# Optimization experiments

Hardware: AMD Instinct MI355X
Metric: run time of the kernel (lower is better)

## Reference

```python
import jax, jax.numpy as jnp
import numpy as np

B, T, H = 2048, 2048, 32  # batch, sequence steps (columns of input), hidden size


def setup_inputs() -> dict:
    key = jax.random.key(0)
    ks = jax.random.split(key, 5)
    stdv = 1.0 / np.sqrt(H)
    u = lambda k, shp: jax.random.uniform(k, shp, jnp.float32, -stdv, stdv)
    return {
        "x": jax.random.normal(ks[0], (B, T), jnp.float32),
        "weight_ih": u(ks[1], (4 * H, 1)),
        "weight_hh": u(ks[2], (4 * H, H)),
        "bias_ih": u(ks[3], (4 * H,)),
        "bias_hh": u(ks[4], (4 * H,)),
    }


def reference(x, weight_ih, weight_hh, bias_ih, bias_hh):
    Bn, Tn = x.shape
    Hn = weight_hh.shape[1]
    xs = x.T[:, :, None]              # (T, B, 1): step-major inputs
    bias = bias_ih + bias_hh          # (4H,)

    def step(carry, x_t):
        h, c = carry                  # (B, H) each
        gates = x_t @ weight_ih.T + h @ weight_hh.T + bias  # (B, 4H)
        i, f, g, o = jnp.split(gates, 4, axis=1)
        i = jax.nn.sigmoid(i)
        f = jax.nn.sigmoid(f)
        g = jnp.tanh(g)
        o = jax.nn.sigmoid(o)
        # row 0 of the original skips the forget term entirely; with c0 = 0,
        # f * c0 == 0, so this is identical math.
        c_new = f * c + i * g
        h_new = o * jnp.tanh(c_new)
        return (h_new, c_new), h_new

    h0 = jnp.zeros((Bn, Hn), x.dtype)
    c0 = jnp.zeros((Bn, Hn), x.dtype)
    _, ys = jax.lax.scan(step, (h0, c0), xs)   # ys: (T, B, H)
    # torch.cat(h_matrix, 1): step-major blocks of width H along dim 1
    return jnp.transpose(ys, (1, 0, 2)).reshape(Bn, Tn * Hn)
```

## Files before the change

### kernel.cpp

```cpp
#include <hip/hip_runtime.h>
#include <hip/hip_fp16.h>


#define Bsz 2048
#define Tsz 2048
#define Hsz 32

typedef _Float16 v2h __attribute__((ext_vector_type(2)));

__device__ __forceinline__ float fast_rcp(float x) { return __builtin_amdgcn_rcpf(x); }
__device__ __forceinline__ float fast_exp2(float x) { return __builtin_amdgcn_exp2f(x); }

__device__ __forceinline__ float fdot2(unsigned a, unsigned b, float c) {
#if __has_builtin(__builtin_amdgcn_fdot2)
    return __builtin_amdgcn_fdot2(__builtin_bit_cast(v2h, a),
                                  __builtin_bit_cast(v2h, b), c, false);
#else
    v2h av = __builtin_bit_cast(v2h, a), bv = __builtin_bit_cast(v2h, b);
    return __fmaf_rn((float)av.x, (float)bv.x,
                     __fmaf_rn((float)av.y, (float)bv.y, c));
#endif
}

__device__ __forceinline__ void plswap(float a, float b, float& r0, float& r1) {
#if __has_builtin(__builtin_amdgcn_permlane32_swap)
    auto r = __builtin_amdgcn_permlane32_swap(__float_as_uint(a), __float_as_uint(b),
                                              false, false);
    r0 = __uint_as_float(r[0]);
    r1 = __uint_as_float(r[1]);
#else
    const bool hi = (threadIdx.x & 32) != 0;
    r0 = hi ? __shfl_xor(b, 32) : a;
    r1 = hi ? b : __shfl_xor(a, 32);
#endif
}

__device__ __forceinline__ unsigned pkh(float a, float b) {
    unsigned ua = (unsigned)__builtin_bit_cast(unsigned short, (_Float16)a);
    unsigned ub = (unsigned)__builtin_bit_cast(unsigned short, (_Float16)b);
    return ua | (ub << 16);
}

__global__ void lstm_prep_kernel(const float* __restrict__ w_ih,
                                 const float* __restrict__ w_hh,
                                 const float* __restrict__ b_ih,
                                 const float* __restrict__ b_hh,
                                 unsigned* __restrict__ ws) {
    const int t = threadIdx.x;
#pragma unroll
    for (int i = t; i < 2048; i += 256) {
        const int q = i >> 8;
        const int l = (i >> 2) & 63;
        const int d = i & 3;
        const int m = (q & 3) * 4 + d;
        const int j = (l >> 5) * 64 + (l & 31) + ((q >> 2) ? 32 : 0);
        ws[i] = pkh(w_hh[j * 32 + 2 * m], w_hh[j * 32 + 2 * m + 1]);
    }
    if (t < 64) {
        const int jA = (t >> 5) * 64 + (t & 31), jB = jA + 32;
        float4 v;
        v.x = w_ih[jA]; v.y = b_ih[jA] + b_hh[jA];
        v.z = w_ih[jB]; v.w = b_ih[jB] + b_hh[jB];
        reinterpret_cast<float4*>(ws + 2048)[t] = v;
    }
}

__global__ __launch_bounds__(256)
__attribute__((amdgpu_waves_per_eu(2, 2)))
void lstm_fwd_kernel(
    const float* __restrict__ x,
    const unsigned* __restrict__ ws,
    float* __restrict__ out)
{
    __shared__ _Float16 hbuf[4][32];

    const int lane = threadIdx.x & 63;
    const int k    = lane & 31;
    const int gp   = lane >> 5;
    const int wv   = __builtin_amdgcn_readfirstlane((int)(threadIdx.x >> 6));
    const int b    = blockIdx.x * 4 + wv;

    unsigned WA[16], WB[16];
    {
        const uint4* wq = reinterpret_cast<const uint4*>(ws) + lane;
#pragma unroll
        for (int q = 0; q < 4; ++q) {
            uint4 u = wq[q * 64];
            WA[4 * q] = u.x; WA[4 * q + 1] = u.y; WA[4 * q + 2] = u.z; WA[4 * q + 3] = u.w;
        }
#pragma unroll
        for (int q = 0; q < 4; ++q) {
            uint4 u = wq[(4 + q) * 64];
            WB[4 * q] = u.x; WB[4 * q + 1] = u.y; WB[4 * q + 2] = u.z; WB[4 * q + 3] = u.w;
        }
    }
    asm volatile("" : "+v"(WA[0]), "+v"(WA[1]), "+v"(WA[2]), "+v"(WA[3]),
                      "+v"(WA[4]), "+v"(WA[5]), "+v"(WA[6]), "+v"(WA[7]));
    asm volatile("" : "+v"(WA[8]), "+v"(WA[9]), "+v"(WA[10]), "+v"(WA[11]),
                      "+v"(WA[12]), "+v"(WA[13]), "+v"(WA[14]), "+v"(WA[15]));
    asm volatile("" : "+v"(WB[0]), "+v"(WB[1]), "+v"(WB[2]), "+v"(WB[3]),
                      "+v"(WB[4]), "+v"(WB[5]), "+v"(WB[6]), "+v"(WB[7]));
    asm volatile("" : "+v"(WB[8]), "+v"(WB[9]), "+v"(WB[10]), "+v"(WB[11]),
                      "+v"(WB[12]), "+v"(WB[13]), "+v"(WB[14]), "+v"(WB[15]));

    const float4 wb = reinterpret_cast<const float4*>(ws + 2048)[lane];
    const float wiA = wb.x, bsA = wb.y, wiB = wb.z, bsB = wb.w;

    const float B1 = gp ? -2.885390082f : -1.442695041f;
    const float A1 = gp ? 2.0f : 1.0f;
    const float C1 = gp ? -1.0f : 0.0f;

    float c = 0.0f, h = 0.0f, hprev = 0.0f;
    hbuf[wv][k] = (_Float16)0.0f;

    const float* xrow = x + (size_t)b * Tsz;
    float* op = out + (size_t)b * (size_t)(Tsz * Hsz) + gp * 32 + k;
    const uint4* hl = reinterpret_cast<const uint4*>(&hbuf[wv][0]);

    float xc[8], xn[8];
#pragma unroll
    for (int j = 0; j < 8; ++j) xc[j] = xrow[j];

#pragma unroll 1
    for (int t0 = 0; t0 < Tsz; t0 += 8) {
        const int tn = (t0 + 8 < Tsz) ? (t0 + 8) : t0;
#pragma unroll
        for (int j = 0; j < 8; ++j) xn[j] = xrow[tn + j];

#pragma unroll
        for (int u = 0; u < 8; ++u) {
            uint4 q0 = hl[0], q1 = hl[1], q2 = hl[2], q3 = hl[3];
            const unsigned hh[16] = {q0.x, q0.y, q0.z, q0.w,
                                     q1.x, q1.y, q1.z, q1.w,
                                     q2.x, q2.y, q2.z, q2.w,
                                     q3.x, q3.y, q3.z, q3.w};
            const float xt = xc[u];

            float sA0 = 0.f, sA1 = 0.f, sB0 = 0.f, sB1 = 0.f;
#pragma unroll
            for (int m = 0; m < 8; ++m) {
                sA0 = fdot2(hh[m], WA[m], sA0);
                sB0 = fdot2(hh[m], WB[m], sB0);
            }
#pragma unroll
            for (int m = 8; m < 16; ++m) {
                sA1 = fdot2(hh[m], WA[m], sA1);
                sB1 = fdot2(hh[m], WB[m], sB1);
            }
            const float pA = (sA0 + sA1) + __fmaf_rn(wiA, xt, bsA);
            const float pB = (sB0 + sB1) + __fmaf_rn(wiB, xt, bsB);

            const float a1 = __fmaf_rn(A1, fast_rcp(1.0f + fast_exp2(B1 * pA)), C1);
            const float a2 = fast_rcp(1.0f + fast_exp2(-1.442695041f * pB));

            float i_, g_, f_, o_;
            plswap(a1, a1, i_, g_);
            plswap(a2, a2, f_, o_);

            c = __fmaf_rn(f_, c, i_ * g_);
            const float th =
                __fmaf_rn(2.0f, fast_rcp(1.0f + fast_exp2(-2.885390082f * c)), -1.0f);
            h = o_ * th;

            hbuf[wv][k] = (_Float16)h;

            if (u & 1) {
                *op = gp ? h : hprev;
                op += 64;
            } else {
                hprev = h;
            }
        }
#pragma unroll
        for (int j = 0; j < 8; ++j) xc[j] = xn[j];
    }
}

extern "C" void kernel_launch(void* const* d_in, const int* in_sizes, int n_in,
                              void* d_out, int out_size, void* d_ws, size_t ws_size,
                              hipStream_t stream) {
    const float* x    = (const float*)d_in[0];
    const float* w_ih = (const float*)d_in[1];
    const float* w_hh = (const float*)d_in[2];
    const float* b_ih = (const float*)d_in[3];
    const float* b_hh = (const float*)d_in[4];
    float* out   = (float*)d_out;
    unsigned* ws = (unsigned*)d_ws;

    lstm_prep_kernel<<<1, 256, 0, stream>>>(w_ih, w_hh, b_ih, b_hh, ws);

    dim3 grid(Bsz / 4);
    dim3 block(256);
    lstm_fwd_kernel<<<grid, block, 0, stream>>>(x, ws, out);
}
```

Measured before the change: 632.5 us.

## Broadcast hidden state via permlane16 swap and DPP rotates instead of LDS

```diff
diff --git a/kernel.cpp b/kernel.cpp
--- a/kernel.cpp
+++ b/kernel.cpp
@@ -35,50 +35,79 @@
 #endif
 }
 
+__device__ __forceinline__ void pl16(unsigned a, unsigned b, unsigned& r0, unsigned& r1) {
+#if __has_builtin(__builtin_amdgcn_permlane16_swap)
+    auto r = __builtin_amdgcn_permlane16_swap(a, b, false, false);
+    r0 = r[0];
+    r1 = r[1];
+#else
+    const bool hi = (threadIdx.x & 16) != 0;
+    r0 = hi ? (unsigned)__shfl_xor((int)a, 16) : a;
+    r1 = hi ? b : (unsigned)__shfl_xor((int)b, 16);
+#endif
+}
+
+template <int N>
+__device__ __forceinline__ unsigned ror16(unsigned v) {
+    if constexpr (N == 0) return v;
+    else
+        return (unsigned)__builtin_amdgcn_mov_dpp((int)v, 0x120 + N, 0xf, 0xf, false);
+}
+
 __device__ __forceinline__ unsigned pkh(float a, float b) {
     unsigned ua = (unsigned)__builtin_bit_cast(unsigned short, (_Float16)a);
     unsigned ub = (unsigned)__builtin_bit_cast(unsigned short, (_Float16)b);
     return ua | (ub << 16);
 }
+
+#define BUILD16(ARR, SRC)                                                    \
+    ARR[0]  = SRC;            ARR[1]  = ror16<1>(SRC);                       \
+    ARR[2]  = ror16<2>(SRC);  ARR[3]  = ror16<3>(SRC);                       \
+    ARR[4]  = ror16<4>(SRC);  ARR[5]  = ror16<5>(SRC);                       \
+    ARR[6]  = ror16<6>(SRC);  ARR[7]  = ror16<7>(SRC);                       \
+    ARR[8]  = ror16<8>(SRC);  ARR[9]  = ror16<9>(SRC);                       \
+    ARR[10] = ror16<10>(SRC); ARR[11] = ror16<11>(SRC);                      \
+    ARR[12] = ror16<12>(SRC); ARR[13] = ror16<13>(SRC);                      \
+    ARR[14] = ror16<14>(SRC); ARR[15] = ror16<15>(SRC);
 
 __global__ void lstm_prep_kernel(const float* __restrict__ w_ih,
                                  const float* __restrict__ w_hh,
                                  const float* __restrict__ b_ih,
                                  const float* __restrict__ b_hh,
                                  unsigned* __restrict__ ws) {
-    const int t = threadIdx.x;
-#pragma unroll
-    for (int i = t; i < 2048; i += 256) {
-        const int q = i >> 8;
-        const int l = (i >> 2) & 63;
-        const int d = i & 3;
-        const int m = (q & 3) * 4 + d;
-        const int j = (l >> 5) * 64 + (l & 31) + ((q >> 2) ? 32 : 0);
-        ws[i] = pkh(w_hh[j * 32 + 2 * m], w_hh[j * 32 + 2 * m + 1]);
+    const int lane = threadIdx.x & 63;
+    unsigned pa, pb;
+    pl16((unsigned)lane, (unsigned)lane, pa, pb);
+    const unsigned probe0 = (pa & 0xffffu) | (pb << 16);
+    unsigned pd[16];
+    BUILD16(pd, probe0)
+
+    const int k = lane & 31, gp = lane >> 5;
+    const int jA = gp * 64 + k, jB = jA + 32;
+    const float* rA = w_hh + (size_t)jA * Hsz;
+    const float* rB = w_hh + (size_t)jB * Hsz;
+#pragma unroll
+    for (int d = 0; d < 16; ++d) {
+        const int ia = (int)(pd[d] & 31u);
+        const int ib = (int)((pd[d] >> 16) & 31u);
+        ws[(d >> 2) * 256 + lane * 4 + (d & 3)]       = pkh(rA[ia], rA[ib]);
+        ws[((d >> 2) + 4) * 256 + lane * 4 + (d & 3)] = pkh(rB[ia], rB[ib]);
     }
-    if (t < 64) {
-        const int jA = (t >> 5) * 64 + (t & 31), jB = jA + 32;
-        float4 v;
-        v.x = w_ih[jA]; v.y = b_ih[jA] + b_hh[jA];
-        v.z = w_ih[jB]; v.w = b_ih[jB] + b_hh[jB];
-        reinterpret_cast<float4*>(ws + 2048)[t] = v;
-    }
-}
-
-__global__ __launch_bounds__(256)
-__attribute__((amdgpu_waves_per_eu(2, 2)))
-void lstm_fwd_kernel(
+    float4 v;
+    v.x = w_ih[jA]; v.y = b_ih[jA] + b_hh[jA];
+    v.z = w_ih[jB]; v.w = b_ih[jB] + b_hh[jB];
+    reinterpret_cast<float4*>(ws + 2048)[lane] = v;
+}
+
+__global__ __launch_bounds__(256, 2) void lstm_fwd_kernel(
     const float* __restrict__ x,
     const unsigned* __restrict__ ws,
     float* __restrict__ out)
 {
-    __shared__ _Float16 hbuf[4][32];
-
     const int lane = threadIdx.x & 63;
     const int k    = lane & 31;
     const int gp   = lane >> 5;
-    const int wv   = __builtin_amdgcn_readfirstlane((int)(threadIdx.x >> 6));
-    const int b    = blockIdx.x * 4 + wv;
+    const int b    = blockIdx.x * 4 + (threadIdx.x >> 6);
 
     unsigned WA[16], WB[16];
     {
@@ -111,11 +140,9 @@
     const float C1 = gp ? -1.0f : 0.0f;
 
     float c = 0.0f, h = 0.0f, hprev = 0.0f;
-    hbuf[wv][k] = (_Float16)0.0f;
 
     const float* xrow = x + (size_t)b * Tsz;
     float* op = out + (size_t)b * (size_t)(Tsz * Hsz) + gp * 32 + k;
-    const uint4* hl = reinterpret_cast<const uint4*>(&hbuf[wv][0]);
 
     float xc[8], xn[8];
 #pragma unroll
@@ -129,24 +156,26 @@
 
 #pragma unroll
         for (int u = 0; u < 8; ++u) {
-            uint4 q0 = hl[0], q1 = hl[1], q2 = hl[2], q3 = hl[3];
-            const unsigned hh[16] = {q0.x, q0.y, q0.z, q0.w,
-                                     q1.x, q1.y, q1.z, q1.w,
-                                     q2.x, q2.y, q2.z, q2.w,
-                                     q3.x, q3.y, q3.z, q3.w};
+            const unsigned hbits =
+                (unsigned)__builtin_bit_cast(unsigned short, (_Float16)h);
+            unsigned ra, rb;
+            pl16(hbits, hbits, ra, rb);
+            const unsigned D0 = (ra & 0xffffu) | (rb << 16);
+            unsigned D[16];
+            BUILD16(D, D0)
+
+            float sA0 = 0.f, sA1 = 0.f, sB0 = 0.f, sB1 = 0.f;
+#pragma unroll
+            for (int m = 0; m < 8; ++m) {
+                sA0 = fdot2(D[m], WA[m], sA0);
+                sB0 = fdot2(D[m], WB[m], sB0);
+            }
+#pragma unroll
+            for (int m = 8; m < 16; ++m) {
+                sA1 = fdot2(D[m], WA[m], sA1);
+                sB1 = fdot2(D[m], WB[m], sB1);
+            }
             const float xt = xc[u];
-
-            float sA0 = 0.f, sA1 = 0.f, sB0 = 0.f, sB1 = 0.f;
-#pragma unroll
-            for (int m = 0; m < 8; ++m) {
-                sA0 = fdot2(hh[m], WA[m], sA0);
-                sB0 = fdot2(hh[m], WB[m], sB0);
-            }
-#pragma unroll
-            for (int m = 8; m < 16; ++m) {
-                sA1 = fdot2(hh[m], WA[m], sA1);
-                sB1 = fdot2(hh[m], WB[m], sB1);
-            }
             const float pA = (sA0 + sA1) + __fmaf_rn(wiA, xt, bsA);
             const float pB = (sB0 + sB1) + __fmaf_rn(wiB, xt, bsB);
 
@@ -161,8 +190,6 @@
             const float th =
                 __fmaf_rn(2.0f, fast_rcp(1.0f + fast_exp2(-2.885390082f * c)), -1.0f);
             h = o_ * th;
-
-            hbuf[wv][k] = (_Float16)h;
 
             if (u & 1) {
                 *op = gp ? h : hprev;
@@ -187,7 +214,7 @@
     float* out   = (float*)d_out;
     unsigned* ws = (unsigned*)d_ws;
 
-    lstm_prep_kernel<<<1, 256, 0, stream>>>(w_ih, w_hh, b_ih, b_hh, ws);
+    lstm_prep_kernel<<<1, 64, 0, stream>>>(w_ih, w_hh, b_ih, b_hh, ws);
 
     dim3 grid(Bsz / 4);
     dim3 block(256);
```

After: 737.2 us. 1.17x slower.
